# Kernel optimization log

Measured on AMD Instinct MI355X. Metric: run time of the kernel, lower is better.

Reference implementation:

```python
import jax, jax.numpy as jnp
import numpy as np
import math

TOPK = 13
NC = 80
ALPHA = 1.0
BETA = 6.0
EPS = 1e-9


def _xyxy2wh(b):
    return b[..., 2:4] - b[..., 0:2]


def _bbox_ciou(box1, box2, eps=1e-7):
    # box1: [bs,nmax,1,4] gt, box2: [bs,1,na,4] pred, xyxy. Returns [bs,nmax,na].
    b1x1, b1y1, b1x2, b1y2 = jnp.split(box1, 4, axis=-1)
    b2x1, b2y1, b2x2, b2y2 = jnp.split(box2, 4, axis=-1)
    w1, h1 = b1x2 - b1x1, b1y2 - b1y1 + eps
    w2, h2 = b2x2 - b2x1, b2y2 - b2y1 + eps
    inter = jnp.clip(jnp.minimum(b1x2, b2x2) - jnp.maximum(b1x1, b2x1), 0) * \
            jnp.clip(jnp.minimum(b1y2, b2y2) - jnp.maximum(b1y1, b2y1), 0)
    union = w1 * h1 + w2 * h2 - inter + eps
    iou = inter / union
    cw = jnp.maximum(b1x2, b2x2) - jnp.minimum(b1x1, b2x1)  # enclosing box
    ch = jnp.maximum(b1y2, b2y2) - jnp.minimum(b1y1, b2y1)
    c2 = cw ** 2 + ch ** 2 + eps
    rho2 = ((b2x1 + b2x2 - b1x1 - b1x2) ** 2 + (b2y1 + b2y2 - b1y1 - b1y2) ** 2) / 4.0
    v = (4.0 / math.pi ** 2) * (jnp.arctan(w2 / h2) - jnp.arctan(w1 / h1)) ** 2
    a = jax.lax.stop_gradient(v / (v - iou + (1.0 + eps)))  # torch.no_grad alpha
    return (iou - (rho2 / c2 + v * a))[..., 0]


def tal_forward(pd_scores, pd_bboxes, anc_points, gt_labels, gt_bboxes, mask_gt,
                gt_kkpts, pd_kkpts, sigma, stride_tensor, reg_max):
    bs, na, nc = pd_scores.shape
    nmax = gt_bboxes.shape[1]
    dt = pd_scores.dtype
    mgt = mask_gt[..., 0]  # [bs,nmax]

    # --- select_candidates_in_gts: anchor center strictly inside gt box ---
    lt = gt_bboxes[:, :, None, :2]              # [bs,nmax,1,2]
    rb = gt_bboxes[:, :, None, 2:]
    anc = anc_points[None, None]                # [1,1,na,2]
    deltas = jnp.concatenate([anc - lt, rb - anc], -1)  # [bs,nmax,na,4]
    mask_in_gts = (deltas.min(-1) > EPS).astype(dt)

    # --- my_filter_anchor: anchor max predictable box edge >= gt mean edge ---
    aps_max = stride_tensor[:, 0] * (reg_max - 1) * 2          # [na]
    gt_size = _xyxy2wh(gt_bboxes).mean(-1)                     # [bs,nmax] (w+h)/2
    filt = (aps_max[None, None, :] - gt_size[..., None] >= EPS).astype(dt)
    mask_in_gts = mask_in_gts * filt

    m = mask_in_gts * mask_gt  # [bs,nmax,na] float 0/1 (mask_in_gts * mask_gt)

    # --- get_box_metrics ---
    lbl = gt_labels[..., 0].astype(jnp.int32)                  # [bs,nmax]
    onehot = jax.nn.one_hot(lbl, nc, dtype=dt)
    bbox_scores = jnp.einsum('bnc,bgc->bgn', pd_scores, onehot) * m

    iou = jnp.clip(_bbox_ciou(gt_bboxes[:, :, None, :], pd_bboxes[:, None, :, :]), 0)

    # OKS-style keypoint iou (my_kpt_iou)
    area = (_xyxy2wh(gt_bboxes).prod(-1) * 0.53)[:, :, None, None]   # [bs,nmax,1,1]
    kmask = (gt_kkpts[..., 2] != 0)[:, :, None, :].astype(dt)        # [bs,nmax,1,nk]
    d = (pd_kkpts[:, None, :, :, 0] - gt_kkpts[:, :, None, :, 0]) ** 2 + \
        (pd_kkpts[:, None, :, :, 1] - gt_kkpts[:, :, None, :, 1]) ** 2  # [bs,nmax,na,nk]
    e = d / ((2.0 * sigma) ** 2) / (area + 1e-7) / 2.0
    kpt_iou = (jnp.exp(-e) * kmask).sum(-1) / (kmask.sum(-1) + 1e-7)
    kpt_iou = jnp.clip(kpt_iou, 0)

    overlaps = ((iou + kpt_iou) / 2.0) * m
    align_metric = (bbox_scores ** ALPHA) * (overlaps ** BETA)

    # --- select_topk_candidates ---
    topk_mask = jnp.broadcast_to(mgt[:, :, None] > 0, (bs, nmax, TOPK))
    _, idxs = jax.lax.top_k(align_metric, TOPK)                # [bs,nmax,TOPK]
    idxs = jnp.where(topk_mask, idxs, 0)
    flat = idxs.reshape(bs * nmax, TOPK)
    cnt = jnp.zeros((bs * nmax, na), jnp.int32).at[
        jnp.arange(bs * nmax)[:, None], flat].add(1)
    cnt = cnt.reshape(bs, nmax, na)
    mask_topk = jnp.where(cnt > 1, 0, cnt).astype(dt)          # drop duplicated idx 0

    mask_pos = mask_topk * mask_in_gts * mask_gt

    # --- select_highest_overlaps ---
    fg = mask_pos.sum(-2)                                      # [bs,na]
    multi = fg[:, None, :] > 1
    is_max = jax.nn.one_hot(overlaps.argmax(1), nmax, dtype=dt).transpose(0, 2, 1)
    mask_pos = jnp.where(multi, is_max, mask_pos)
    fg = mask_pos.sum(-2)
    tgi = mask_pos.argmax(-2)                                  # [bs,na] target gt idx

    # --- get_targets ---
    flat_idx = tgi + jnp.arange(bs, dtype=tgi.dtype)[:, None] * nmax
    tlabels = jnp.clip(gt_labels.reshape(-1)[flat_idx], 0)     # [bs,na]
    tbboxes = gt_bboxes.reshape(-1, 4)[flat_idx]               # [bs,na,4]
    tscores = jax.nn.one_hot(tlabels, nc, dtype=dt)
    tscores = jnp.where(fg[..., None] > 0, tscores, 0.0)

    # --- normalize scores by aligned metric ---
    align_metric = align_metric * mask_pos
    pos_align = align_metric.max(-1, keepdims=True)            # [bs,nmax,1]
    pos_ov = (overlaps * mask_pos).max(-1, keepdims=True)
    norm = (align_metric * pos_ov / (pos_align + EPS)).max(-2)[..., None]  # [bs,na,1]
    tscores = tscores * norm
    return tlabels, tbboxes, tscores, fg > 0, tgi


def setup_inputs() -> dict:
    key = jax.random.key(0)
    ks = jax.random.split(key, 10)
    bs, nmax, nc, nk = 16, 64, 80, 1
    pts, strs = [], []
    for s, n in [(8, 80), (16, 40), (32, 20)]:
        g = (jnp.arange(n, dtype=jnp.float32) + 0.5) * s
        yv, xv = jnp.meshgrid(g, g, indexing='ij')
        pts.append(jnp.stack([xv.ravel(), yv.ravel()], -1))
        strs.append(jnp.full((n * n, 1), float(s), jnp.float32))
    anc_points = jnp.concatenate(pts, 0)        # [8400,2]
    stride_tensor = jnp.concatenate(strs, 0)    # [8400,1]
    na = anc_points.shape[0]

    def boxes(k, shape):
        k1, k2 = jax.random.split(k)
        c = jax.random.uniform(k1, shape + (2,), jnp.float32, 60.0, 580.0)
        wh = jax.random.uniform(k2, shape + (2,), jnp.float32, 10.0, 120.0)
        return jnp.concatenate([c - wh / 2, c + wh / 2], -1)

    pd_scores = jax.random.uniform(ks[0], (bs, na, nc), jnp.float32)
    pd_bboxes = boxes(ks[1], (bs, na))
    gt_bboxes = boxes(ks[2], (bs, nmax))
    gt_labels = jax.random.randint(ks[3], (bs, nmax, 1), 0, nc)
    mask_gt = (jax.random.uniform(ks[4], (bs, nmax, 1)) < 0.7).astype(jnp.float32)
    gt_xy = jax.random.uniform(ks[5], (bs, nmax, nk, 2), jnp.float32, 0.0, 640.0)
    gt_v = jax.random.randint(ks[6], (bs, nmax, nk, 1), 0, 3).astype(jnp.float32)
    gt_kkpts = jnp.concatenate([gt_xy, gt_v], -1)
    pd_xy = jax.random.uniform(ks[7], (bs, na, nk, 2), jnp.float32, 0.0, 640.0)
    pd_v = jax.random.uniform(ks[8], (bs, na, nk, 1), jnp.float32)
    pd_kkpts = jnp.concatenate([pd_xy, pd_v], -1)
    sigma = jnp.full((nk,), 0.25, jnp.float32)
    return dict(pd_scores=pd_scores, pd_bboxes=pd_bboxes, anc_points=anc_points,
                gt_labels=gt_labels, gt_bboxes=gt_bboxes, mask_gt=mask_gt,
                gt_kkpts=gt_kkpts, pd_kkpts=pd_kkpts, sigma=sigma,
                stride_tensor=stride_tensor, reg_max=16)


def reference(pd_scores, pd_bboxes, anc_points, gt_labels, gt_bboxes, mask_gt,
              gt_kkpts, pd_kkpts, sigma, stride_tensor, reg_max):
    return tal_forward(pd_scores, pd_bboxes, anc_points, gt_labels, gt_bboxes,
                       mask_gt, gt_kkpts, pd_kkpts, sigma, stride_tensor, reg_max)
```

## Files before the change

kernel.cpp:

```cpp
#include <hip/hip_runtime.h>
#include <math.h>
#include <float.h>
#include <limits.h>

#define TOPK 13
typedef unsigned int u32;
typedef unsigned long long u64;

__device__ __forceinline__ u32 q32f(double x) {
  if (!(x > 0.0)) return 0u;
  float f = (float)x;
  u32 b = __float_as_uint(f);
  return (b >= 0x00800000u) ? b : 0u;
}
__device__ __forceinline__ double val32(u32 b) {
  return (double)__uint_as_float(b);
}

struct MetricQ { u32 amb; u32 ovb; bool m; };

__device__ MetricQ metric_at(
    const float* __restrict__ pd_scores, const float* __restrict__ pd_bboxes,
    const float* __restrict__ anc, const int* __restrict__ gt_labels,
    const float* __restrict__ gt_bboxes, const float* __restrict__ mask_gt,
    const float* __restrict__ gt_kkpts, const float* __restrict__ pd_kkpts,
    const float* __restrict__ sigma, const float* __restrict__ stride_t,
    int reg_max, int b, int g, int a, int nmax, int na, int nc, int nk)
{
#pragma clang fp contract(off)
  MetricQ r; r.amb = 0u; r.ovb = 0u; r.m = false;
  const float* gb = gt_bboxes + (size_t)(b * nmax + g) * 4;
  float gx1 = gb[0], gy1 = gb[1], gx2 = gb[2], gy2 = gb[3];
  float mgt = mask_gt[b * nmax + g];
  float ax = anc[(size_t)a * 2 + 0], ay = anc[(size_t)a * 2 + 1];
  float dmin = fminf(fminf(ax - gx1, ay - gy1), fminf(gx2 - ax, gy2 - ay));
  float aps = (stride_t[a] * (float)(reg_max - 1)) * 2.0f;
  float gw = gx2 - gx1, gh = gy2 - gy1;
  float gsize = (gw + gh) * 0.5f;
  bool mm = ((double)dmin > 1e-9) && ((double)(aps - gsize) >= 1e-9) && (mgt > 0.f);
  r.m = mm;
  if (!mm) return r;

  int lbl = gt_labels[b * nmax + g];
  float score = pd_scores[((size_t)(b * na + a)) * nc + lbl];

  const float* pb = pd_bboxes + ((size_t)(b * na + a)) * 4;
  float px1 = pb[0], py1 = pb[1], px2 = pb[2], py2 = pb[3];
  const float e7 = 1e-7f;
  float w1 = gx2 - gx1, h1 = (gy2 - gy1) + e7;
  float w2 = px2 - px1, h2 = (py2 - py1) + e7;
  float iw = fmaxf(fminf(gx2, px2) - fmaxf(gx1, px1), 0.f);
  float ih = fmaxf(fminf(gy2, py2) - fmaxf(gy1, py1), 0.f);
  float inter = iw * ih;
  float uni = ((w1 * h1 + w2 * h2) - inter) + e7;
  float iou = inter / uni;
  float cw = fmaxf(gx2, px2) - fminf(gx1, px1);
  float ch = fmaxf(gy2, py2) - fminf(gy1, py1);
  float c2 = (cw * cw + ch * ch) + e7;
  float dcx = ((px1 + px2) - gx1) - gx2;
  float dcy = ((py1 + py2) - gy1) - gy2;
  float rho2 = (dcx * dcx + dcy * dcy) / 4.0f;
  float a2 = (float)atan((double)(w2 / h2));
  float a1 = (float)atan((double)(w1 / h1));
  float arc = a2 - a1;
  const float C = (float)(4.0 / (3.14159265358979323846 * 3.14159265358979323846));
  float v = C * (arc * arc);
  const float C1 = (float)(1.0 + 1e-7);
  float al = v / ((v - iou) + C1);
  float ciou = iou - (rho2 / c2 + v * al);
  float iouc = fmaxf(ciou, 0.f);

  float area = (gw * gh) * 0.53f;
  double ksum = 0.0;
  float  kcnt = 0.f;
  for (int k = 0; k < nk; k++) {
    const float* gk = gt_kkpts + ((size_t)(b * nmax + g) * nk + k) * 3;
    const float* pk = pd_kkpts + (((size_t)(b * na + a)) * nk + k) * 3;
    float km = (gk[2] != 0.f) ? 1.f : 0.f;
    float dx = pk[0] - gk[0], dy = pk[1] - gk[1];
    float d  = dx * dx + dy * dy;
    float s2 = 2.f * sigma[k]; s2 = s2 * s2;
    float e1 = d / s2;
    float e2 = e1 / (area + 1e-7f);
    float e  = e2 / 2.0f;
    double s1 = val32(q32f(exp(-(double)e)));
    double term = s1 * (double)km;
    ksum = val32(q32f(ksum + term));
    kcnt = kcnt + km;
  }
  double den = (double)(kcnt + 1e-7f);
  u32 kioub = q32f(ksum / den);
  double kiou = val32(kioub);
  u32 sumb = q32f((double)iouc + kiou);
  u32 ovlb = q32f(val32(sumb) * 0.5);
  double ovl = val32(ovlb);
  u32 p6b = q32f(pow(ovl, 6.0));
  u32 amb = q32f((double)score * val32(p6b));
  r.ovb = ovlb;
  r.amb = amb;
  return r;
}

__global__ void k_zero4(float* __restrict__ p, long n4) {
  long i = (long)blockIdx.x * blockDim.x + threadIdx.x;
  if (i < n4) ((float4*)p)[i] = make_float4(0.f, 0.f, 0.f, 0.f);
}
__global__ void k_zeroi(int* __restrict__ p, long n) {
  long i = (long)blockIdx.x * blockDim.x + threadIdx.x;
  if (i < n) p[i] = 0;
}

#define MAXC 512

__global__ void k_rows(const float* __restrict__ pd_scores, const float* __restrict__ pd_bboxes,
                       const float* __restrict__ anc, const int* __restrict__ gt_labels,
                       const float* __restrict__ gt_bboxes, const float* __restrict__ mask_gt,
                       const float* __restrict__ gt_kkpts, const float* __restrict__ pd_kkpts,
                       const float* __restrict__ sigma, const float* __restrict__ stride_t,
                       const int* __restrict__ reg_max_p,
                       int* __restrict__ cnt, int* __restrict__ gsel,
                       u32* __restrict__ amsel, u32* __restrict__ ovsel,
                       int bs, int nmax, int na, int nc, int nk)
{
  int g = blockIdx.x, b = blockIdx.y;
  if (mask_gt[b * nmax + g] <= 0.f) return;
  int reg_max = reg_max_p[0];
  int tid = threadIdx.x;
  int wave = tid >> 6, lane = tid & 63;

  __shared__ int   s_ncand;
  __shared__ int   s_cand[MAXC];
  __shared__ u32   s_keyv[MAXC];
  __shared__ u32   s_ovv[MAXC];
  __shared__ unsigned short s_ciOf[1024];
  __shared__ u32   s_bitPos[32];
  __shared__ u64   s_red[4];
  __shared__ u64   s_win;
  __shared__ int   s_selA[TOPK];
  __shared__ int   s_selCi[TOPK];

  if (tid == 0) s_ncand = 0;
  if (tid < 32) s_bitPos[tid] = 0u;
  for (int i = tid; i < 1024; i += 256) s_ciOf[i] = 0xFFFF;
  __syncthreads();

  {
    const float* gb = gt_bboxes + (size_t)(b * nmax + g) * 4;
    float gx1 = gb[0], gy1 = gb[1], gx2 = gb[2], gy2 = gb[3];
    float gw = gx2 - gx1, gh = gy2 - gy1;
    float gsize = (gw + gh) * 0.5f;
    for (int a = tid; a < na; a += 256) {
      float ax = anc[(size_t)a * 2 + 0], ay = anc[(size_t)a * 2 + 1];
      float dmin = fminf(fminf(ax - gx1, ay - gy1), fminf(gx2 - ax, gy2 - ay));
      float aps = (stride_t[a] * (float)(reg_max - 1)) * 2.0f;
      bool mm = ((double)dmin > 1e-9) && ((double)(aps - gsize) >= 1e-9);
      if (mm) {
        int ci = atomicAdd(&s_ncand, 1);
        if (ci < MAXC) {
          s_cand[ci] = a;
          if (a < 1024) s_ciOf[a] = (unsigned short)ci;
        }
      }
    }
  }
  __syncthreads();
  int ncand = min(s_ncand, MAXC);

  for (int ci = tid; ci < ncand; ci += 256) {
    int a = s_cand[ci];
    MetricQ mt = metric_at(pd_scores, pd_bboxes, anc, gt_labels, gt_bboxes, mask_gt,
                           gt_kkpts, pd_kkpts, sigma, stride_t, reg_max,
                           b, g, a, nmax, na, nc, nk);
    s_keyv[ci] = mt.amb;
    s_ovv[ci]  = mt.ovb;
    if (mt.amb != 0u && a < 1024) atomicOr(&s_bitPos[a >> 5], 1u << (a & 31));
  }
  __syncthreads();

  u32 pk = 0xFFFFFFFFu; int pi = -1;
  int npos = TOPK;
  for (int k = 0; k < TOPK; k++) {
    u32 bK = 0u; int bA = INT_MAX; int bCi = -1;
    for (int ci = tid; ci < ncand; ci += 256) {
      u32 vv = s_keyv[ci]; int a = s_cand[ci];
      if (vv < pk || (vv == pk && a > pi)) {
        if (vv > bK || (vv == bK && a < bA)) { bK = vv; bA = a; bCi = ci; }
      }
    }
    u64 p = ((u64)bK << 32) | (u64)(u32)(0xFFFFFFFFu - (u32)bA);
    for (int off = 32; off; off >>= 1) {
      u64 q = __shfl_xor(p, off);
      if (q > p) p = q;
    }
    if (lane == 0) s_red[wave] = p;
    __syncthreads();
    if (tid == 0) {
      u64 w = s_red[0];
      for (int i = 1; i < 4; i++) if (s_red[i] > w) w = s_red[i];
      s_win = w;
    }
    __syncthreads();
    u64 win = s_win;
    u32 wK = (u32)(win >> 32);
    if (wK == 0u) { npos = k; break; }
    int wA = (int)(0xFFFFFFFFu - (u32)(win & 0xFFFFFFFFu));
    if (p == win && bCi >= 0 && bK == wK && bA == wA) {
      s_selCi[k] = bCi; s_selA[k] = wA;
    }
    pk = wK; pi = wA;
    __syncthreads();
  }

  __syncthreads();
  if (tid == 0) {
    int a = 0;
    for (int k = npos; k < TOPK; k++) {
      while ((s_bitPos[a >> 5] >> (a & 31)) & 1u) a++;
      s_selA[k] = a;
      s_selCi[k] = (s_ciOf[a] == 0xFFFF) ? -1 : (int)s_ciOf[a];
      a++;
    }
  }
  __syncthreads();

  if (tid < TOPK) {
    int ci = s_selCi[tid];
    if (ci >= 0) {
      int a = s_selA[tid];
      int t = b * na + a;
      atomicAdd(&cnt[t], 1);
      gsel[t] = g;
      amsel[t] = s_keyv[ci];
      ovsel[t] = s_ovv[ci];
    }
  }
}

__global__ void k_anchors(const int* __restrict__ gt_labels, const float* __restrict__ gt_bboxes,
                          const int* __restrict__ cnt, const int* __restrict__ gsel,
                          const u32* __restrict__ amsel, const u32* __restrict__ ovsel,
                          u32* __restrict__ pa, u32* __restrict__ po,
                          u32* __restrict__ amfin, float* __restrict__ out,
                          int* __restrict__ mcount, int* __restrict__ mlist,
                          int bs, int nmax, int na, int nc,
                          long tb_off, long fg_off, long tgi_off)
{
  int t = blockIdx.x * blockDim.x + threadIdx.x;
  if (t >= bs * na) return;
  int b = t / na;

  int c = cnt[t];
  if (c > 1) {
    int i = atomicAdd(mcount, 1);
    mlist[i] = t;
    return;
  }
  int tgi = 0; u32 amb = 0u, ovb = 0u; bool fg = false;
  if (c == 1) { tgi = gsel[t]; amb = amsel[t]; ovb = ovsel[t]; fg = true; }

  int lbl = gt_labels[b * nmax + tgi]; if (lbl < 0) lbl = 0;
  out[t] = (float)lbl;
  const float* gb = gt_bboxes + (size_t)(b * nmax + tgi) * 4;
  float* tb = out + tb_off + (long)t * 4;
  tb[0] = gb[0]; tb[1] = gb[1]; tb[2] = gb[2]; tb[3] = gb[3];
  out[fg_off + t] = fg ? 1.0f : 0.0f;
  out[tgi_off + t] = (float)tgi;

  amfin[t] = amb;
  if (fg) {
    int row = b * nmax + tgi;
    atomicMax(&pa[row], amb);
    atomicMax(&po[row], ovb);
  }
}

__global__ void k_multi(const float* __restrict__ pd_scores, const float* __restrict__ pd_bboxes,
                        const float* __restrict__ anc, const int* __restrict__ gt_labels,
                        const float* __restrict__ gt_bboxes, const float* __restrict__ mask_gt,
                        const float* __restrict__ gt_kkpts, const float* __restrict__ pd_kkpts,
                        const float* __restrict__ sigma, const float* __restrict__ stride_t,
                        const int* __restrict__ reg_max_p,
                        const int* __restrict__ mcount, const int* __restrict__ mlist,
                        u32* __restrict__ pa, u32* __restrict__ po,
                        u32* __restrict__ amfin, float* __restrict__ out,
                        int bs, int nmax, int na, int nc, int nk,
                        long tb_off, long fg_off, long tgi_off)
{
  int waveId = (int)((blockIdx.x * blockDim.x + threadIdx.x) >> 6);
  int lane   = threadIdx.x & 63;
  int nwaves = (int)((gridDim.x * blockDim.x) >> 6);
  int reg_max = reg_max_p[0];
  int M = mcount[0];

  for (int i = waveId; i < M; i += nwaves) {
    int t = mlist[i];
    int b = t / na, a = t - b * na;
    u32 ovg = 0u, amg = 0u;
    if (lane < nmax) {
      MetricQ mt = metric_at(pd_scores, pd_bboxes, anc, gt_labels, gt_bboxes, mask_gt,
                             gt_kkpts, pd_kkpts, sigma, stride_t, reg_max,
                             b, lane, a, nmax, na, nc, nk);
      ovg = mt.m ? mt.ovb : 0u;
      amg = mt.m ? mt.amb : 0u;
    }
    u64 p = ((u64)ovg << 32) | (u64)(u32)(0xFFFFFFFFu - (u32)lane);
    for (int off = 32; off; off >>= 1) {
      u64 q = __shfl_xor(p, off);
      if (q > p) p = q;
    }
    int wg = (int)(0xFFFFFFFFu - (u32)(p & 0xFFFFFFFFu));
    if (lane == wg) {
      int lbl = gt_labels[b * nmax + wg]; if (lbl < 0) lbl = 0;
      out[t] = (float)lbl;
      const float* gb = gt_bboxes + (size_t)(b * nmax + wg) * 4;
      float* tb = out + tb_off + (long)t * 4;
      tb[0] = gb[0]; tb[1] = gb[1]; tb[2] = gb[2]; tb[3] = gb[3];
      out[fg_off + t] = 1.0f;
      out[tgi_off + t] = (float)wg;
      amfin[t] = amg;
      int row = b * nmax + wg;
      atomicMax(&pa[row], amg);
      atomicMax(&po[row], ovg);
    }
  }
}

__global__ void k_scores(const u32* __restrict__ pa, const u32* __restrict__ po,
                         const u32* __restrict__ amfin, float* __restrict__ out,
                         int bs, int nmax, int na, int nc, long ts_off, long fg_off, long tgi_off)
{
  int t = blockIdx.x * blockDim.x + threadIdx.x;
  if (t >= bs * na) return;
  if (out[fg_off + t] <= 0.f) return;
  int b = t / na;
  int tgi = (int)out[tgi_off + t];
  int row = b * nmax + tgi;
  u32 rb = q32f(val32(po[row]) / (val32(pa[row]) + (double)1e-9f));
  u32 nb = q32f(val32(amfin[t]) * val32(rb));
  int lbl = (int)out[t];
  out[ts_off + (long)t * nc + lbl] = __uint_as_float(nb);
}

extern "C" void kernel_launch(void* const* d_in, const int* in_sizes, int n_in,
                              void* d_out, int out_size, void* d_ws, size_t ws_size,
                              hipStream_t stream) {
  const float* pd_scores = (const float*)d_in[0];
  const float* pd_bboxes = (const float*)d_in[1];
  const float* anc       = (const float*)d_in[2];
  const int*   gt_labels = (const int*)  d_in[3];
  const float* gt_bboxes = (const float*)d_in[4];
  const float* mask_gt   = (const float*)d_in[5];
  const float* gt_kkpts  = (const float*)d_in[6];
  const float* pd_kkpts  = (const float*)d_in[7];
  const float* sigma     = (const float*)d_in[8];
  const float* stride_t  = (const float*)d_in[9];
  const int*   reg_max_p = (const int*)  d_in[10];

  int na   = in_sizes[2] / 2;
  int bs   = in_sizes[1] / (na * 4);
  int nc   = in_sizes[0] / (bs * na);
  int nmax = in_sizes[3] / bs;
  int nk   = in_sizes[8];

  long nba = (long)bs * na;
  int  R   = bs * nmax;

  int* cnt    = (int*)d_ws;
  u32* pa     = (u32*)(cnt + nba);
  u32* po     = pa + R;
  int* mcount = (int*)(po + R);
  int* gsel   = mcount + 64;
  u32* amsel  = (u32*)(gsel + nba);
  u32* ovsel  = amsel + nba;
  u32* amfin  = ovsel + nba;
  int* mlist  = (int*)(amfin + nba);

  float* out = (float*)d_out;
  long tb_off  = nba;
  long ts_off  = nba * 5;
  long fg_off  = ts_off + nba * nc;
  long tgi_off = fg_off + nba;

  long nz = nba + 2L * R + 64;
  k_zeroi<<<(int)((nz + 255) / 256), 256, 0, stream>>>(cnt, nz);
  long n4 = (nba * nc) / 4;
  k_zero4<<<(int)((n4 + 255) / 256), 256, 0, stream>>>(out + ts_off, n4);

  dim3 grows(nmax, bs);
  k_rows<<<grows, 256, 0, stream>>>(pd_scores, pd_bboxes, anc, gt_labels, gt_bboxes,
                                    mask_gt, gt_kkpts, pd_kkpts, sigma, stride_t,
                                    reg_max_p, cnt, gsel, amsel, ovsel,
                                    bs, nmax, na, nc, nk);

  int nthr = (int)((nba + 255) / 256);
  k_anchors<<<nthr, 256, 0, stream>>>(gt_labels, gt_bboxes, cnt, gsel, amsel, ovsel,
                                      pa, po, amfin, out, mcount, mlist,
                                      bs, nmax, na, nc, tb_off, fg_off, tgi_off);

  k_multi<<<256, 256, 0, stream>>>(pd_scores, pd_bboxes, anc, gt_labels, gt_bboxes,
                                   mask_gt, gt_kkpts, pd_kkpts, sigma, stride_t,
                                   reg_max_p, mcount, mlist, pa, po, amfin, out,
                                   bs, nmax, na, nc, nk, tb_off, fg_off, tgi_off);

  k_scores<<<nthr, 256, 0, stream>>>(pa, po, amfin, out, bs, nmax, na, nc,
                                     ts_off, fg_off, tgi_off);
}
```

Before: 158.9 us.

## Fuse score zeroing into scatter kernel and use single-wave register top-k

Removes the separate zero-fill kernel for the dense target-score tensor; k_scores now writes each anchor's whole score row itself, emitting zeros plus the one labelled value with float4 stores. Top-k selection in k_rows becomes a single wave holding up to 512 candidate keys in registers, which removes the per-iteration block barriers and shared-memory reductions. Anchor points are read as float2. This saves a full pass over the largest output and the barrier-heavy selection loop, but the wave-only top-k relies on ncand never exceeding 512, which holds because MAXC is 512.

```diff
diff --git a/kernel.cpp b/kernel.cpp
--- a/kernel.cpp
+++ b/kernel.cpp
@@ -101,10 +101,6 @@
   return r;
 }
 
-__global__ void k_zero4(float* __restrict__ p, long n4) {
-  long i = (long)blockIdx.x * blockDim.x + threadIdx.x;
-  if (i < n4) ((float4*)p)[i] = make_float4(0.f, 0.f, 0.f, 0.f);
-}
 __global__ void k_zeroi(int* __restrict__ p, long n) {
   long i = (long)blockIdx.x * blockDim.x + threadIdx.x;
   if (i < n) p[i] = 0;
@@ -134,8 +130,6 @@
   __shared__ u32   s_ovv[MAXC];
   __shared__ unsigned short s_ciOf[1024];
   __shared__ u32   s_bitPos[32];
-  __shared__ u64   s_red[4];
-  __shared__ u64   s_win;
   __shared__ int   s_selA[TOPK];
   __shared__ int   s_selCi[TOPK];
 
@@ -149,9 +143,10 @@
     float gx1 = gb[0], gy1 = gb[1], gx2 = gb[2], gy2 = gb[3];
     float gw = gx2 - gx1, gh = gy2 - gy1;
     float gsize = (gw + gh) * 0.5f;
+    const float2* anc2 = (const float2*)anc;
     for (int a = tid; a < na; a += 256) {
-      float ax = anc[(size_t)a * 2 + 0], ay = anc[(size_t)a * 2 + 1];
-      float dmin = fminf(fminf(ax - gx1, ay - gy1), fminf(gx2 - ax, gy2 - ay));
+      float2 av = anc2[a];
+      float dmin = fminf(fminf(av.x - gx1, av.y - gy1), fminf(gx2 - av.x, gy2 - av.y));
       float aps = (stride_t[a] * (float)(reg_max - 1)) * 2.0f;
       bool mm = ((double)dmin > 1e-9) && ((double)(aps - gsize) >= 1e-9);
       if (mm) {
@@ -177,48 +172,44 @@
   }
   __syncthreads();
 
-  u32 pk = 0xFFFFFFFFu; int pi = -1;
-  int npos = TOPK;
-  for (int k = 0; k < TOPK; k++) {
-    u32 bK = 0u; int bA = INT_MAX; int bCi = -1;
-    for (int ci = tid; ci < ncand; ci += 256) {
-      u32 vv = s_keyv[ci]; int a = s_cand[ci];
-      if (vv < pk || (vv == pk && a > pi)) {
-        if (vv > bK || (vv == bK && a < bA)) { bK = vv; bA = a; bCi = ci; }
+  if (wave == 0) {
+    u64 kk[8];
+#pragma unroll
+    for (int j = 0; j < 8; j++) {
+      int ci = lane + (j << 6);
+      u64 v = 0;
+      if (ci < ncand) {
+        u32 amb = s_keyv[ci];
+        if (amb != 0u)
+          v = ((u64)amb << 32) | (u64)(u32)(0xFFFFFFFFu - (u32)s_cand[ci]);
       }
-    }
-    u64 p = ((u64)bK << 32) | (u64)(u32)(0xFFFFFFFFu - (u32)bA);
-    for (int off = 32; off; off >>= 1) {
-      u64 q = __shfl_xor(p, off);
-      if (q > p) p = q;
-    }
-    if (lane == 0) s_red[wave] = p;
-    __syncthreads();
-    if (tid == 0) {
-      u64 w = s_red[0];
-      for (int i = 1; i < 4; i++) if (s_red[i] > w) w = s_red[i];
-      s_win = w;
-    }
-    __syncthreads();
-    u64 win = s_win;
-    u32 wK = (u32)(win >> 32);
-    if (wK == 0u) { npos = k; break; }
-    int wA = (int)(0xFFFFFFFFu - (u32)(win & 0xFFFFFFFFu));
-    if (p == win && bCi >= 0 && bK == wK && bA == wA) {
-      s_selCi[k] = bCi; s_selA[k] = wA;
-    }
-    pk = wK; pi = wA;
-    __syncthreads();
-  }
-
-  __syncthreads();
-  if (tid == 0) {
-    int a = 0;
-    for (int k = npos; k < TOPK; k++) {
-      while ((s_bitPos[a >> 5] >> (a & 31)) & 1u) a++;
-      s_selA[k] = a;
-      s_selCi[k] = (s_ciOf[a] == 0xFFFF) ? -1 : (int)s_ciOf[a];
-      a++;
+      kk[j] = v;
+    }
+    int np = TOPK;
+    for (int k = 0; k < TOPK; k++) {
+      u64 best = 0; int bj = 0;
+#pragma unroll
+      for (int j = 0; j < 8; j++) if (kk[j] > best) { best = kk[j]; bj = j; }
+      u64 p = best;
+      for (int off = 32; off; off >>= 1) {
+        u64 q = __shfl_xor(p, off);
+        if (q > p) p = q;
+      }
+      if ((u32)(p >> 32) == 0u) { np = k; break; }
+      if (best == p) {
+        s_selA[k]  = (int)(0xFFFFFFFFu - (u32)p);
+        s_selCi[k] = lane + (bj << 6);
+        kk[bj] = 0;
+      }
+    }
+    if (lane == 0) {
+      int a = 0;
+      for (int k = np; k < TOPK; k++) {
+        while ((s_bitPos[a >> 5] >> (a & 31)) & 1u) a++;
+        s_selA[k] = a;
+        s_selCi[k] = (s_ciOf[a] == 0xFFFF) ? -1 : (int)s_ciOf[a];
+        a++;
+      }
     }
   }
   __syncthreads();
@@ -329,16 +320,51 @@
                          const u32* __restrict__ amfin, float* __restrict__ out,
                          int bs, int nmax, int na, int nc, long ts_off, long fg_off, long tgi_off)
 {
-  int t = blockIdx.x * blockDim.x + threadIdx.x;
-  if (t >= bs * na) return;
-  if (out[fg_off + t] <= 0.f) return;
-  int b = t / na;
-  int tgi = (int)out[tgi_off + t];
-  int row = b * nmax + tgi;
-  u32 rb = q32f(val32(po[row]) / (val32(pa[row]) + (double)1e-9f));
-  u32 nb = q32f(val32(amfin[t]) * val32(rb));
-  int lbl = (int)out[t];
-  out[ts_off + (long)t * nc + lbl] = __uint_as_float(nb);
+  __shared__ float s_val[64];
+  __shared__ int   s_lbl[64];
+  long nba = (long)bs * na;
+  long base = (long)blockIdx.x * 64;
+  int tid = threadIdx.x;
+
+  if (tid < 64) {
+    long t = base + tid;
+    float v = 0.f; int lbl = 0;
+    if (t < nba && out[fg_off + t] > 0.f) {
+      int b = (int)(t / na);
+      int tgi = (int)out[tgi_off + t];
+      int row = b * nmax + tgi;
+      u32 rb = q32f(val32(po[row]) / (val32(pa[row]) + (double)1e-9f));
+      u32 nb = q32f(val32(amfin[t]) * val32(rb));
+      v = __uint_as_float(nb);
+      lbl = (int)out[t];
+    }
+    s_val[tid] = v; s_lbl[tid] = lbl;
+  }
+  __syncthreads();
+
+  int nA = (int)min((long)64, nba - base);
+  if (nA <= 0) return;
+
+  if ((nc & 3) == 0) {
+    int nc4 = nc >> 2;
+    float4* dst = (float4*)(out + ts_off + base * nc);
+    int total = nA * nc4;
+    for (int q = tid; q < total; q += 256) {
+      int aIdx = q / nc4, c4 = (q - aIdx * nc4) << 2;
+      float v = s_val[aIdx]; int lbl = s_lbl[aIdx];
+      float4 o = make_float4(0.f, 0.f, 0.f, 0.f);
+      int d = lbl - c4;
+      if (d >= 0 && d < 4) ((float*)&o)[d] = v;
+      dst[q] = o;
+    }
+  } else {
+    float* dst = out + ts_off + base * nc;
+    int total = nA * nc;
+    for (int q = tid; q < total; q += 256) {
+      int aIdx = q / nc, c = q - aIdx * nc;
+      dst[q] = (c == s_lbl[aIdx]) ? s_val[aIdx] : 0.f;
+    }
+  }
 }
 
 extern "C" void kernel_launch(void* const* d_in, const int* in_sizes, int n_in,
@@ -383,8 +409,6 @@
 
   long nz = nba + 2L * R + 64;
   k_zeroi<<<(int)((nz + 255) / 256), 256, 0, stream>>>(cnt, nz);
-  long n4 = (nba * nc) / 4;
-  k_zero4<<<(int)((n4 + 255) / 256), 256, 0, stream>>>(out + ts_off, n4);
 
   dim3 grows(nmax, bs);
   k_rows<<<grows, 256, 0, stream>>>(pd_scores, pd_bboxes, anc, gt_labels, gt_bboxes,
@@ -402,6 +426,7 @@
                                    reg_max_p, mcount, mlist, pa, po, amfin, out,
                                    bs, nmax, na, nc, nk, tb_off, fg_off, tgi_off);
 
-  k_scores<<<nthr, 256, 0, stream>>>(pa, po, amfin, out, bs, nmax, na, nc,
-                                     ts_off, fg_off, tgi_off);
-}
+  int nblk_s = (int)((nba + 63) / 64);
+  k_scores<<<nblk_s, 256, 0, stream>>>(pa, po, amfin, out, bs, nmax, na, nc,
+                                       ts_off, fg_off, tgi_off);
+}
```

After: 163.1 us. +2.7%, slower.
